# Kernel tuning notes

Measured on AMD Instinct MI355X. Metric: run time of the kernel, lower is better.

## Reference

```python
import jax, jax.numpy as jnp
import numpy as np

BANDS = np.array([0, 1, 2, 3, 4])
LOG_STDEVS = (0.0, 1.0)
CLAHE_MIN_STDEV = 1.0
K = 9      # CLAHE kernel size (hardcoded in module)
PAD = 4    # CLAHE reflect padding (hardcoded in module)


def _box_mean(x):
    # x: [B, C, H, W]; mean over KxK sliding window with reflect padding,
    # identical math to torch Unfold + mean over the K*K window axis.
    p = jnp.pad(x, ((0, 0), (0, 0), (PAD, PAD), (PAD, PAD)), mode='reflect')
    s = jax.lax.reduce_window(p, jnp.float32(0.0), jax.lax.add,
                              (1, 1, K, K), (1, 1, 1, 1), 'VALID')
    return s / (K * K)


def _clahe(img5d, min_stdev):
    # img5d: [B, C, 1, H, W]
    x = img5d[:, :, 0]
    res = x - _box_mean(x)
    stdev = jnp.sqrt(_box_mean(res * res))
    return (res / jnp.maximum(stdev, min_stdev))[:, :, None]


def setup_inputs() -> dict:
    key = jax.random.key(0)
    k1, k2 = jax.random.split(key, 2)
    B, C, H, W = 8, 5, 512, 512
    T = 3
    images = jax.random.normal(k1, (B, C, H, W), jnp.float32) * 10.0 + 100.0
    # background must be positive (asserted > 1e-6 in the module)
    background = jax.random.uniform(k2, (B, C, H, W), jnp.float32) * 50.0 + 50.0
    # learnable asinh params, initialized exactly as in __init__
    asinh_thresholds = jnp.tile(
        jnp.array([0.0, 1.0, 10.0], jnp.float32).reshape(1, 1, T, 1, 1),
        (1, C, 1, 1, 1))
    asinh_scales = jnp.full((1, C, T, 1, 1), np.log(0.1), jnp.float32)
    return {'images': images, 'background': background,
            'asinh_thresholds': asinh_thresholds, 'asinh_scales': asinh_scales}


def reference(images, background, asinh_thresholds, asinh_scales):
    raw = images[:, BANDS][:, :, None]        # [B, C, 1, H, W]
    bg = background[:, BANDS][:, :, None]     # [B, C, 1, H, W]
    inputs = [raw]                            # include_original=True; asinh on -> no raw background channel
    for t in LOG_STDEVS:
        off = (raw - bg) / jnp.sqrt(bg) - t
        inputs.append(jnp.log(jnp.maximum(off + 1.0, 1.0)))
    inputs.append(_clahe(raw, CLAHE_MIN_STDEV))
    inputs.append(jnp.arcsinh((raw - asinh_thresholds) * jnp.exp(asinh_scales)))
    return jnp.concatenate(inputs, axis=2)    # [B, C, 7, H, W]
```

## Files before the change

kernel.cpp:

```cpp
#include <hip/hip_runtime.h>
#include <math.h>

#define IMG_H 512
#define IMG_W 512
#define TS 32
#define NC 5
#define NB 8

__device__ __forceinline__ int reflect_idx(int i, int n) {
    if (i < 0) i = -i;
    if (i >= n) i = 2 * n - 2 - i;
    return i;
}

__device__ __forceinline__ float fast_log(float x) {
    return __builtin_amdgcn_logf(x) * 0.6931471805599453f;
}

__device__ __forceinline__ float fast_asinh(float v) {
    float a = fabsf(v);
    float r = fast_log(a + __builtin_amdgcn_sqrtf(fmaf(a, a, 1.0f)));
    return copysignf(r, v);
}

__global__ __launch_bounds__(256)
void imnorm_kernel(const float* __restrict__ img, const float* __restrict__ bgr,
                   const float* __restrict__ thr, const float* __restrict__ scl,
                   float* __restrict__ out)
{
    const int plane = blockIdx.z;
    const int c = plane % NC;
    const int h0 = blockIdx.y * TS;
    const int w0 = blockIdx.x * TS;
    const bool edge_w = (w0 == 0) || (w0 + TS == IMG_W);
    const bool edge_h = (h0 == 0) || (h0 + TS == IMG_H);

    const float* x  = img + (size_t)plane * IMG_H * IMG_W;
    const float* bg = bgr + (size_t)plane * IMG_H * IMG_W;
    float* op = out + (size_t)plane * 7 * IMG_H * IMG_W;

    const int t = threadIdx.y * 32 + threadIdx.x;

    __shared__ float xs[48][52];
    __shared__ float rs[40][44];
    __shared__ float pool[48 * 41];
    float (*h1)[41] = reinterpret_cast<float (*)[41]>(pool);
    float (*v2)[44] = reinterpret_cast<float (*)[44]>(pool);

    const int r5  = t >> 3;
    const int wl0 = (t & 7) * 4;

    const float4 bgv = *reinterpret_cast<const float4*>(
        bg + (size_t)(h0 + r5) * IMG_W + (w0 + wl0));

    float s_thr[3], s_exp[3];
    #pragma unroll
    for (int j = 0; j < 3; ++j) {
        s_thr[j] = thr[c * 3 + j];
        s_exp[j] = __builtin_amdgcn_exp2f(scl[c * 3 + j] * 1.4426950408889634f);
    }

    if (!edge_w && !edge_h) {
        const float4* src4 = reinterpret_cast<const float4*>(
            x + (size_t)(h0 - 8) * IMG_W + (w0 - 8));
        #pragma unroll
        for (int k = 0; k < 3; ++k) {
            int i = t + k * 256;
            if (i < 576) {
                int r = i / 12, cc = i - r * 12;
                *reinterpret_cast<float4*>(&xs[r][cc * 4]) = src4[r * 128 + cc];
            }
        }
    } else {
        #pragma unroll
        for (int k = 0; k < 9; ++k) {
            int i = t + k * 256;
            int r = i / 48, cc = i - r * 48;
            int gr = reflect_idx(h0 - 8 + r, IMG_H);
            int gc = reflect_idx(w0 - 8 + cc, IMG_W);
            xs[r][cc] = x[gr * IMG_W + gc];
        }
    }
    __syncthreads();

    if (t < 240) {
        const int r  = t / 5;
        const int c0 = (t - r * 5) * 8;
        float s = xs[r][c0];
        #pragma unroll
        for (int d = 1; d < 9; ++d) s += xs[r][c0 + d];
        h1[r][c0] = s;
        #pragma unroll
        for (int k = 1; k < 8; ++k) {
            s += xs[r][c0 + 8 + k] - xs[r][c0 + k - 1];
            h1[r][c0 + k] = s;
        }
    }
    __syncthreads();

    if (t < 200) {
        const int seg = t / 40;
        const int cl  = t - seg * 40;
        const int r0  = seg * 8;
        float s = h1[r0][cl];
        #pragma unroll
        for (int d = 1; d < 9; ++d) s += h1[r0 + d][cl];
        rs[r0][cl] = xs[r0 + 4][cl + 4] - s * (1.0f / 81.0f);
        #pragma unroll
        for (int k = 1; k < 8; ++k) {
            s += h1[r0 + 8 + k][cl] - h1[r0 + k - 1][cl];
            rs[r0 + k][cl] = xs[r0 + k + 4][cl + 4] - s * (1.0f / 81.0f);
        }
    }
    __syncthreads();

    if (t < 160) {
        const int seg = t / 40;
        const int cl  = t - seg * 40;
        const int r0  = seg * 8;
        if (!edge_h) {
            float v = rs[r0][cl];
            float s = v * v;
            #pragma unroll
            for (int d = 1; d < 9; ++d) { v = rs[r0 + d][cl]; s = fmaf(v, v, s); }
            v2[r0][cl] = s;
            #pragma unroll
            for (int k = 1; k < 8; ++k) {
                float a = rs[r0 + 8 + k][cl];
                float b = rs[r0 + k - 1][cl];
                s = fmaf(a, a, fmaf(b, -b, s));
                v2[r0 + k][cl] = s;
            }
        } else {
            #pragma unroll
            for (int k = 0; k < 8; ++k) {
                const int hh = h0 + r0 + k;
                float s = 0.f;
                #pragma unroll
                for (int d = 0; d < 9; ++d) {
                    int mr = reflect_idx(hh - 4 + d, IMG_H) - (h0 - 4);
                    float v = rs[mr][cl];
                    s = fmaf(v, v, s);
                }
                v2[r0 + k][cl] = s;
            }
        }
    }
    __syncthreads();

    float ssum[4];
    if (!edge_w) {
        const float* vr = &v2[r5][wl0];
        float4 A  = *reinterpret_cast<const float4*>(vr);
        float4 Bv = *reinterpret_cast<const float4*>(vr + 4);
        float4 Cv = *reinterpret_cast<const float4*>(vr + 8);
        float s0 = ((A.x + A.y) + (A.z + A.w)) + ((Bv.x + Bv.y) + (Bv.z + Bv.w)) + Cv.x;
        ssum[0] = s0;
        ssum[1] = s0      - A.x + Cv.y;
        ssum[2] = ssum[1] - A.y + Cv.z;
        ssum[3] = ssum[2] - A.z + Cv.w;
    } else {
        #pragma unroll
        for (int j = 0; j < 4; ++j) {
            const int w = w0 + wl0 + j;
            float s = 0.f;
            #pragma unroll
            for (int d = 0; d < 9; ++d) {
                int mc = reflect_idx(w - 4 + d, IMG_W) - (w0 - 4);
                s += v2[r5][mc];
            }
            ssum[j] = s;
        }
    }

    const float4 rsv = *reinterpret_cast<const float4*>(&rs[r5 + 4][wl0 + 4]);
    const float4 xsv = *reinterpret_cast<const float4*>(&xs[r5 + 8][wl0 + 8]);

    float o_raw[4], o_l0[4], o_l1[4], o_cl[4], o_a0[4], o_a1[4], o_a2[4];
    const float rsa[4] = {rsv.x, rsv.y, rsv.z, rsv.w};
    const float xsa[4] = {xsv.x, xsv.y, xsv.z, xsv.w};
    const float bga[4] = {bgv.x, bgv.y, bgv.z, bgv.w};

    #pragma unroll
    for (int j = 0; j < 4; ++j) {
        float stdev = __builtin_amdgcn_sqrtf(fmaxf(ssum[j], 0.0f) * (1.0f / 81.0f));
        o_cl[j] = rsa[j] * __builtin_amdgcn_rcpf(fmaxf(stdev, 1.0f));

        float raw = xsa[j];
        o_raw[j] = raw;
        float off0 = (raw - bga[j]) * __builtin_amdgcn_rsqf(bga[j]);
        o_l0[j] = fast_log(fmaxf(off0 + 1.0f, 1.0f));
        o_l1[j] = fast_log(fmaxf(off0, 1.0f));
        o_a0[j] = fast_asinh((raw - s_thr[0]) * s_exp[0]);
        o_a1[j] = fast_asinh((raw - s_thr[1]) * s_exp[1]);
        o_a2[j] = fast_asinh((raw - s_thr[2]) * s_exp[2]);
    }

    const size_t chs = (size_t)IMG_H * IMG_W;
    float* p = op + (size_t)(h0 + r5) * IMG_W + (w0 + wl0);
    *reinterpret_cast<float4*>(p) = make_float4(o_raw[0], o_raw[1], o_raw[2], o_raw[3]); p += chs;
    *reinterpret_cast<float4*>(p) = make_float4(o_l0[0],  o_l0[1],  o_l0[2],  o_l0[3]);  p += chs;
    *reinterpret_cast<float4*>(p) = make_float4(o_l1[0],  o_l1[1],  o_l1[2],  o_l1[3]);  p += chs;
    *reinterpret_cast<float4*>(p) = make_float4(o_cl[0],  o_cl[1],  o_cl[2],  o_cl[3]);  p += chs;
    *reinterpret_cast<float4*>(p) = make_float4(o_a0[0],  o_a0[1],  o_a0[2],  o_a0[3]);  p += chs;
    *reinterpret_cast<float4*>(p) = make_float4(o_a1[0],  o_a1[1],  o_a1[2],  o_a1[3]);  p += chs;
    *reinterpret_cast<float4*>(p) = make_float4(o_a2[0],  o_a2[1],  o_a2[2],  o_a2[3]);
}

extern "C" void kernel_launch(void* const* d_in, const int* in_sizes, int n_in,
                              void* d_out, int out_size, void* d_ws, size_t ws_size,
                              hipStream_t stream) {
    const float* img = (const float*)d_in[0];
    const float* bg  = (const float*)d_in[1];
    const float* thr = (const float*)d_in[2];
    const float* scl = (const float*)d_in[3];
    float* out = (float*)d_out;

    dim3 grid(IMG_W / TS, IMG_H / TS, NB * NC);
    dim3 block(32, 8);
    hipLaunchKernelGGL(imnorm_kernel, grid, block, 0, stream,
                       img, bg, thr, scl, out);
}
```

Baseline: 359.0 us.

## Split pointwise channels and CLAHE stencil into separate block groups

```diff
diff --git a/kernel.cpp b/kernel.cpp
--- a/kernel.cpp
+++ b/kernel.cpp
@@ -30,35 +30,64 @@
 {
     const int plane = blockIdx.z;
     const int c = plane % NC;
+    const int bx = blockIdx.x;
+    const int t = threadIdx.y * 32 + threadIdx.x;
+    const size_t chs = (size_t)IMG_H * IMG_W;
+    float* op = out + (size_t)plane * 7 * chs;
+
+    if (bx >= 16) {
+        const int w0s = (bx - 16) * TS;
+        const int h0s = blockIdx.y * TS;
+        const int row = t >> 3;
+        const int col = (t & 7) * 4;
+
+        const size_t base = (size_t)plane * chs + (size_t)(h0s + row) * IMG_W + (w0s + col);
+        const float4 raw4 = *reinterpret_cast<const float4*>(img + base);
+        const float4 bg4  = *reinterpret_cast<const float4*>(bgr + base);
+
+        float s_thr[3], s_exp[3];
+        #pragma unroll
+        for (int j = 0; j < 3; ++j) {
+            s_thr[j] = thr[c * 3 + j];
+            s_exp[j] = __builtin_amdgcn_exp2f(scl[c * 3 + j] * 1.4426950408889634f);
+        }
+
+        const float rawa[4] = {raw4.x, raw4.y, raw4.z, raw4.w};
+        const float bga[4]  = {bg4.x,  bg4.y,  bg4.z,  bg4.w};
+        float o_l0[4], o_l1[4], o_a0[4], o_a1[4], o_a2[4];
+        #pragma unroll
+        for (int j = 0; j < 4; ++j) {
+            float raw  = rawa[j];
+            float off0 = (raw - bga[j]) * __builtin_amdgcn_rsqf(bga[j]);
+            o_l0[j] = fast_log(fmaxf(off0 + 1.0f, 1.0f));
+            o_l1[j] = fast_log(fmaxf(off0, 1.0f));
+            o_a0[j] = fast_asinh((raw - s_thr[0]) * s_exp[0]);
+            o_a1[j] = fast_asinh((raw - s_thr[1]) * s_exp[1]);
+            o_a2[j] = fast_asinh((raw - s_thr[2]) * s_exp[2]);
+        }
+
+        float* p = op + (size_t)(h0s + row) * IMG_W + (w0s + col);
+        *reinterpret_cast<float4*>(p) = raw4;
+        *reinterpret_cast<float4*>(p + 1 * chs) = make_float4(o_l0[0], o_l0[1], o_l0[2], o_l0[3]);
+        *reinterpret_cast<float4*>(p + 2 * chs) = make_float4(o_l1[0], o_l1[1], o_l1[2], o_l1[3]);
+        *reinterpret_cast<float4*>(p + 4 * chs) = make_float4(o_a0[0], o_a0[1], o_a0[2], o_a0[3]);
+        *reinterpret_cast<float4*>(p + 5 * chs) = make_float4(o_a1[0], o_a1[1], o_a1[2], o_a1[3]);
+        *reinterpret_cast<float4*>(p + 6 * chs) = make_float4(o_a2[0], o_a2[1], o_a2[2], o_a2[3]);
+        return;
+    }
+
     const int h0 = blockIdx.y * TS;
-    const int w0 = blockIdx.x * TS;
+    const int w0 = bx * TS;
     const bool edge_w = (w0 == 0) || (w0 + TS == IMG_W);
     const bool edge_h = (h0 == 0) || (h0 + TS == IMG_H);
 
-    const float* x  = img + (size_t)plane * IMG_H * IMG_W;
-    const float* bg = bgr + (size_t)plane * IMG_H * IMG_W;
-    float* op = out + (size_t)plane * 7 * IMG_H * IMG_W;
-
-    const int t = threadIdx.y * 32 + threadIdx.x;
+    const float* x = img + (size_t)plane * chs;
 
     __shared__ float xs[48][52];
     __shared__ float rs[40][44];
     __shared__ float pool[48 * 41];
     float (*h1)[41] = reinterpret_cast<float (*)[41]>(pool);
     float (*v2)[44] = reinterpret_cast<float (*)[44]>(pool);
-
-    const int r5  = t >> 3;
-    const int wl0 = (t & 7) * 4;
-
-    const float4 bgv = *reinterpret_cast<const float4*>(
-        bg + (size_t)(h0 + r5) * IMG_W + (w0 + wl0));
-
-    float s_thr[3], s_exp[3];
-    #pragma unroll
-    for (int j = 0; j < 3; ++j) {
-        s_thr[j] = thr[c * 3 + j];
-        s_exp[j] = __builtin_amdgcn_exp2f(scl[c * 3 + j] * 1.4426950408889634f);
-    }
 
     if (!edge_w && !edge_h) {
         const float4* src4 = reinterpret_cast<const float4*>(
@@ -147,6 +176,9 @@
         }
     }
     __syncthreads();
+
+    const int r5  = t >> 3;
+    const int wl0 = (t & 7) * 4;
 
     float ssum[4];
     if (!edge_w) {
@@ -174,37 +206,16 @@
     }
 
     const float4 rsv = *reinterpret_cast<const float4*>(&rs[r5 + 4][wl0 + 4]);
-    const float4 xsv = *reinterpret_cast<const float4*>(&xs[r5 + 8][wl0 + 8]);
-
-    float o_raw[4], o_l0[4], o_l1[4], o_cl[4], o_a0[4], o_a1[4], o_a2[4];
     const float rsa[4] = {rsv.x, rsv.y, rsv.z, rsv.w};
-    const float xsa[4] = {xsv.x, xsv.y, xsv.z, xsv.w};
-    const float bga[4] = {bgv.x, bgv.y, bgv.z, bgv.w};
-
+    float o_cl[4];
     #pragma unroll
     for (int j = 0; j < 4; ++j) {
         float stdev = __builtin_amdgcn_sqrtf(fmaxf(ssum[j], 0.0f) * (1.0f / 81.0f));
         o_cl[j] = rsa[j] * __builtin_amdgcn_rcpf(fmaxf(stdev, 1.0f));
-
-        float raw = xsa[j];
-        o_raw[j] = raw;
-        float off0 = (raw - bga[j]) * __builtin_amdgcn_rsqf(bga[j]);
-        o_l0[j] = fast_log(fmaxf(off0 + 1.0f, 1.0f));
-        o_l1[j] = fast_log(fmaxf(off0, 1.0f));
-        o_a0[j] = fast_asinh((raw - s_thr[0]) * s_exp[0]);
-        o_a1[j] = fast_asinh((raw - s_thr[1]) * s_exp[1]);
-        o_a2[j] = fast_asinh((raw - s_thr[2]) * s_exp[2]);
-    }
-
-    const size_t chs = (size_t)IMG_H * IMG_W;
-    float* p = op + (size_t)(h0 + r5) * IMG_W + (w0 + wl0);
-    *reinterpret_cast<float4*>(p) = make_float4(o_raw[0], o_raw[1], o_raw[2], o_raw[3]); p += chs;
-    *reinterpret_cast<float4*>(p) = make_float4(o_l0[0],  o_l0[1],  o_l0[2],  o_l0[3]);  p += chs;
-    *reinterpret_cast<float4*>(p) = make_float4(o_l1[0],  o_l1[1],  o_l1[2],  o_l1[3]);  p += chs;
-    *reinterpret_cast<float4*>(p) = make_float4(o_cl[0],  o_cl[1],  o_cl[2],  o_cl[3]);  p += chs;
-    *reinterpret_cast<float4*>(p) = make_float4(o_a0[0],  o_a0[1],  o_a0[2],  o_a0[3]);  p += chs;
-    *reinterpret_cast<float4*>(p) = make_float4(o_a1[0],  o_a1[1],  o_a1[2],  o_a1[3]);  p += chs;
-    *reinterpret_cast<float4*>(p) = make_float4(o_a2[0],  o_a2[1],  o_a2[2],  o_a2[3]);
+    }
+
+    float* p = op + 3 * chs + (size_t)(h0 + r5) * IMG_W + (w0 + wl0);
+    *reinterpret_cast<float4*>(p) = make_float4(o_cl[0], o_cl[1], o_cl[2], o_cl[3]);
 }
 
 extern "C" void kernel_launch(void* const* d_in, const int* in_sizes, int n_in,
@@ -216,7 +227,7 @@
     const float* scl = (const float*)d_in[3];
     float* out = (float*)d_out;
 
-    dim3 grid(IMG_W / TS, IMG_H / TS, NB * NC);
+    dim3 grid(32, IMG_H / TS, NB * NC);
     dim3 block(32, 8);
     hipLaunchKernelGGL(imnorm_kernel, grid, block, 0, stream,
                        img, bg, thr, scl, out);
```

After: 371.6 us. +3.5%, slower.

## Issue pointwise outputs early with nontemporal stores to overlap with box filters

Applied to the files above, without the earlier changes.

```diff
diff --git a/kernel.cpp b/kernel.cpp
--- a/kernel.cpp
+++ b/kernel.cpp
@@ -6,6 +6,9 @@
 #define TS 32
 #define NC 5
 #define NB 8
+#define CHS ((size_t)IMG_H * IMG_W)
+
+typedef float f32x4 __attribute__((ext_vector_type(4)));
 
 __device__ __forceinline__ int reflect_idx(int i, int n) {
     if (i < 0) i = -i;
@@ -21,6 +24,15 @@
     float a = fabsf(v);
     float r = fast_log(a + __builtin_amdgcn_sqrtf(fmaf(a, a, 1.0f)));
     return copysignf(r, v);
+}
+
+__device__ __forceinline__ void nt_store4(float* p, float a, float b, float c, float d) {
+    f32x4 v = {a, b, c, d};
+    __builtin_nontemporal_store(v, reinterpret_cast<f32x4*>(p));
+}
+
+__device__ __forceinline__ f32x4 nt_load4(const float* p) {
+    return __builtin_nontemporal_load(reinterpret_cast<const f32x4*>(p));
 }
 
 __global__ __launch_bounds__(256)
@@ -35,13 +47,13 @@
     const bool edge_w = (w0 == 0) || (w0 + TS == IMG_W);
     const bool edge_h = (h0 == 0) || (h0 + TS == IMG_H);
 
-    const float* x  = img + (size_t)plane * IMG_H * IMG_W;
-    const float* bg = bgr + (size_t)plane * IMG_H * IMG_W;
-    float* op = out + (size_t)plane * 7 * IMG_H * IMG_W;
+    const float* x  = img + plane * CHS;
+    const float* bg = bgr + plane * CHS;
+    float* op = out + plane * 7 * CHS;
 
     const int t = threadIdx.y * 32 + threadIdx.x;
 
-    __shared__ float xs[48][52];
+    __shared__ float xs[48][48];
     __shared__ float rs[40][44];
     __shared__ float pool[48 * 41];
     float (*h1)[41] = reinterpret_cast<float (*)[41]>(pool);
@@ -50,8 +62,7 @@
     const int r5  = t >> 3;
     const int wl0 = (t & 7) * 4;
 
-    const float4 bgv = *reinterpret_cast<const float4*>(
-        bg + (size_t)(h0 + r5) * IMG_W + (w0 + wl0));
+    const f32x4 bgv = nt_load4(bg + (size_t)(h0 + r5) * IMG_W + (w0 + wl0));
 
     float s_thr[3], s_exp[3];
     #pragma unroll
@@ -82,6 +93,30 @@
         }
     }
     __syncthreads();
+
+    {
+        const float4 raw4 = *reinterpret_cast<const float4*>(&xs[r5 + 8][wl0 + 8]);
+        const float rawa[4] = {raw4.x, raw4.y, raw4.z, raw4.w};
+        const float bga[4]  = {bgv.x,  bgv.y,  bgv.z,  bgv.w};
+        float o_l0[4], o_l1[4], o_a0[4], o_a1[4], o_a2[4];
+        #pragma unroll
+        for (int j = 0; j < 4; ++j) {
+            float raw  = rawa[j];
+            float off0 = (raw - bga[j]) * __builtin_amdgcn_rsqf(bga[j]);
+            o_l0[j] = fast_log(fmaxf(off0 + 1.0f, 1.0f));
+            o_l1[j] = fast_log(fmaxf(off0, 1.0f));
+            o_a0[j] = fast_asinh((raw - s_thr[0]) * s_exp[0]);
+            o_a1[j] = fast_asinh((raw - s_thr[1]) * s_exp[1]);
+            o_a2[j] = fast_asinh((raw - s_thr[2]) * s_exp[2]);
+        }
+        float* p = op + (size_t)(h0 + r5) * IMG_W + (w0 + wl0);
+        nt_store4(p,           rawa[0], rawa[1], rawa[2], rawa[3]);
+        nt_store4(p + 1 * CHS, o_l0[0], o_l0[1], o_l0[2], o_l0[3]);
+        nt_store4(p + 2 * CHS, o_l1[0], o_l1[1], o_l1[2], o_l1[3]);
+        nt_store4(p + 4 * CHS, o_a0[0], o_a0[1], o_a0[2], o_a0[3]);
+        nt_store4(p + 5 * CHS, o_a1[0], o_a1[1], o_a1[2], o_a1[3]);
+        nt_store4(p + 6 * CHS, o_a2[0], o_a2[1], o_a2[2], o_a2[3]);
+    }
 
     if (t < 240) {
         const int r  = t / 5;
@@ -174,37 +209,16 @@
     }
 
     const float4 rsv = *reinterpret_cast<const float4*>(&rs[r5 + 4][wl0 + 4]);
-    const float4 xsv = *reinterpret_cast<const float4*>(&xs[r5 + 8][wl0 + 8]);
-
-    float o_raw[4], o_l0[4], o_l1[4], o_cl[4], o_a0[4], o_a1[4], o_a2[4];
     const float rsa[4] = {rsv.x, rsv.y, rsv.z, rsv.w};
-    const float xsa[4] = {xsv.x, xsv.y, xsv.z, xsv.w};
-    const float bga[4] = {bgv.x, bgv.y, bgv.z, bgv.w};
-
+    float o_cl[4];
     #pragma unroll
     for (int j = 0; j < 4; ++j) {
         float stdev = __builtin_amdgcn_sqrtf(fmaxf(ssum[j], 0.0f) * (1.0f / 81.0f));
         o_cl[j] = rsa[j] * __builtin_amdgcn_rcpf(fmaxf(stdev, 1.0f));
-
-        float raw = xsa[j];
-        o_raw[j] = raw;
-        float off0 = (raw - bga[j]) * __builtin_amdgcn_rsqf(bga[j]);
-        o_l0[j] = fast_log(fmaxf(off0 + 1.0f, 1.0f));
-        o_l1[j] = fast_log(fmaxf(off0, 1.0f));
-        o_a0[j] = fast_asinh((raw - s_thr[0]) * s_exp[0]);
-        o_a1[j] = fast_asinh((raw - s_thr[1]) * s_exp[1]);
-        o_a2[j] = fast_asinh((raw - s_thr[2]) * s_exp[2]);
-    }
-
-    const size_t chs = (size_t)IMG_H * IMG_W;
-    float* p = op + (size_t)(h0 + r5) * IMG_W + (w0 + wl0);
-    *reinterpret_cast<float4*>(p) = make_float4(o_raw[0], o_raw[1], o_raw[2], o_raw[3]); p += chs;
-    *reinterpret_cast<float4*>(p) = make_float4(o_l0[0],  o_l0[1],  o_l0[2],  o_l0[3]);  p += chs;
-    *reinterpret_cast<float4*>(p) = make_float4(o_l1[0],  o_l1[1],  o_l1[2],  o_l1[3]);  p += chs;
-    *reinterpret_cast<float4*>(p) = make_float4(o_cl[0],  o_cl[1],  o_cl[2],  o_cl[3]);  p += chs;
-    *reinterpret_cast<float4*>(p) = make_float4(o_a0[0],  o_a0[1],  o_a0[2],  o_a0[3]);  p += chs;
-    *reinterpret_cast<float4*>(p) = make_float4(o_a1[0],  o_a1[1],  o_a1[2],  o_a1[3]);  p += chs;
-    *reinterpret_cast<float4*>(p) = make_float4(o_a2[0],  o_a2[1],  o_a2[2],  o_a2[3]);
+    }
+
+    float* p3 = op + 3 * CHS + (size_t)(h0 + r5) * IMG_W + (w0 + wl0);
+    nt_store4(p3, o_cl[0], o_cl[1], o_cl[2], o_cl[3]);
 }
 
 extern "C" void kernel_launch(void* const* d_in, const int* in_sizes, int n_in,
```

Result: no change. 353.0 us (-1.7%).
